# Performance work log

Hardware: AMD Instinct MI355X
Metric: run time of the kernel (lower is better)

The kernel has to match this reference:

```python
import jax, jax.numpy as jnp
import numpy as np

KS = 3          # deformable kernel size
PAD = 1         # zero padding
N = KS * KS     # sampling points per pixel
INC = 64
OUTC = 64


def _conv(x, w, stride, pad, groups):
    return jax.lax.conv_general_dilated(
        x, w, (stride, stride), ((pad, pad), (pad, pad)),
        feature_group_count=groups,
        dimension_numbers=('NCHW', 'OIHW', 'NCHW'))


def setup_inputs() -> dict:
    key = jax.random.key(0)
    k = jax.random.split(key, 5)
    b, h, w = 4, 128, 128
    x = jax.random.normal(k[0], (b, INC, h, w), jnp.float32)
    # SeparableConv2d params (bias=False throughout in source)
    p_dw = jax.random.normal(k[1], (INC, 1, 3, 3), jnp.float32) * 0.1     # p_conv depthwise 3x3 pad1
    p_pw = jax.random.normal(k[2], (2 * N, INC, 1, 1), jnp.float32) * 0.1  # p_conv pointwise -> 2N offsets
    c_dw = jax.random.normal(k[3], (INC, 1, KS, KS), jnp.float32) * 0.1    # conv depthwise k=ks stride=ks
    c_pw = jax.random.normal(k[4], (OUTC, INC, 1, 1), jnp.float32) * 0.1   # conv pointwise
    return {'x': x, 'p_dw': p_dw, 'p_pw': p_pw, 'c_dw': c_dw, 'c_pw': c_pw}


def reference(x, p_dw, p_pw, c_dw, c_pw):
    b, c, h, w = x.shape
    offset = _conv(_conv(x, p_dw, 1, 1, INC), p_pw, 1, 0, 1)   # [b, 2N, h, w]
    xp = jnp.pad(x, ((0, 0), (0, 0), (PAD, PAD), (PAD, PAD)))  # zero_padding
    Hp, Wp = h + 2 * PAD, w + 2 * PAD
    # p_n: kernel-relative offsets (row-major over ks x ks, 'ij' meshgrid)
    r = jnp.arange(-(KS - 1) // 2, (KS - 1) // 2 + 1, dtype=jnp.float32)
    pnx, pny = jnp.meshgrid(r, r, indexing='ij')
    p_n = jnp.concatenate([pnx.ravel(), pny.ravel()])[None, :, None, None]  # [1, 2N, 1, 1]
    # p_0: base grid, 1-indexed (accounts for padding), stride=1
    gx = jnp.arange(1, h + 1, dtype=jnp.float32)[None, None, :, None]
    gy = jnp.arange(1, w + 1, dtype=jnp.float32)[None, None, None, :]
    p0 = jnp.concatenate([jnp.broadcast_to(gx, (1, N, h, w)),
                          jnp.broadcast_to(gy, (1, N, h, w))], axis=1)      # [1, 2N, h, w]
    p = (p0 + p_n + offset).transpose(0, 2, 3, 1)                           # [b, h, w, 2N]
    px, py = p[..., :N], p[..., N:]
    fx, fy = jnp.floor(px), jnp.floor(py)
    ltx = jnp.clip(fx, 0, Hp - 1); lty = jnp.clip(fy, 0, Wp - 1)
    rbx = jnp.clip(fx + 1, 0, Hp - 1); rby = jnp.clip(fy + 1, 0, Wp - 1)
    pxc = jnp.clip(px, 0, Hp - 1); pyc = jnp.clip(py, 0, Wp - 1)
    # bilinear weights
    g_lt = (1 + (ltx - pxc)) * (1 + (lty - pyc))
    g_rb = (1 - (rbx - pxc)) * (1 - (rby - pyc))
    g_lb = (1 + (ltx - pxc)) * (1 - (rby - pyc))
    g_rt = (1 - (rbx - pxc)) * (1 + (lty - pyc))
    x_flat = xp.reshape(b, c, Hp * Wp)

    def gather(qx, qy):  # -> [b, c, h, w, N]
        idx = (qx * Wp + qy).astype(jnp.int32).reshape(b, 1, h * w * N)
        return jnp.take_along_axis(x_flat, idx, axis=2).reshape(b, c, h, w, N)

    x_off = (g_lt[:, None] * gather(ltx, lty) + g_rb[:, None] * gather(rbx, rby)
             + g_lb[:, None] * gather(ltx, rby) + g_rt[:, None] * gather(rbx, lty))
    # _reshape_x_offset: [b,c,h,w,N] -> [b,c,h*ks,w*ks]
    x_off = x_off.reshape(b, c, h, w, KS, KS).transpose(0, 1, 2, 4, 3, 5).reshape(b, c, h * KS, w * KS)
    # SeparableConv2d(inc, outc, k=ks, stride=ks)
    return _conv(_conv(x_off, c_dw, KS, 0, INC), c_pw, 1, 0, 1)
```

## Files before the change

kernel.cpp:

```cpp
#include <hip/hip_runtime.h>
#include <hip/hip_fp16.h>

#define Hdim 128
#define Wdim 128
#define Cdim 64
#define HW   (Hdim * Wdim)
#define NPIX (4 * HW)
#define NBLK (NPIX / 64)
#define NXCD 8
#define Hp 130
#define HWp (Hp * Hp)

typedef _Float16 v8h __attribute__((ext_vector_type(8)));
typedef float    v4f __attribute__((ext_vector_type(4)));

__device__ __forceinline__ int xcd_swizzle(int bid, int nblk) {
    return (bid % NXCD) * (nblk / NXCD) + bid / NXCD;
}


__global__ __launch_bounds__(512) void offset_geo_kernel(
    const float* __restrict__ x,
    const float* __restrict__ p_dw,
    const float* __restrict__ p_pw,
    __half* __restrict__ xt,
    unsigned int* __restrict__ geo)
{
    __shared__ float part[8][18][64];

    int lane = threadIdx.x & 63;
    int g    = threadIdx.x >> 6;
    int blk  = xcd_swizzle(blockIdx.x, NBLK);
    int pix0 = blk * 64;
    int pix  = pix0 + lane;
    int w = pix & (Wdim - 1);
    int h = (pix >> 7) & (Hdim - 1);
    int b = pix >> 14;

    {
        int gid = blockIdx.x * 512 + threadIdx.x;
        if (gid < 2064 * 8) {
            int rp  = gid >> 3, sub = gid & 7;
            int img = rp / 516, pos = rp - img * 516;
            int i, j;
            if (pos < 130)      { i = 0;   j = pos; }
            else if (pos < 260) { i = 129; j = pos - 130; }
            else { int p2 = pos - 260; i = 1 + (p2 >> 1); j = (p2 & 1) ? 129 : 0; }
            float4* dst = (float4*)(xt + ((size_t)img * HWp + i * Hp + j) * Cdim);
            dst[sub] = make_float4(0.f, 0.f, 0.f, 0.f);
        }
    }

    int   off9[9];
    float msk9[9];
#pragma unroll
    for (int dh = -1; dh <= 1; ++dh) {
#pragma unroll
        for (int dw = -1; dw <= 1; ++dw) {
            int tap = (dh + 1) * 3 + (dw + 1);
            int hh = h + dh, ww = w + dw;
            bool ok = (hh >= 0) & (hh < Hdim) & (ww >= 0) & (ww < Wdim);
            off9[tap] = ok ? hh * Wdim + ww : 0;
            msk9[tap] = ok ? 1.f : 0.f;
        }
    }

    float t[8], ctr[8];
#pragma unroll
    for (int i = 0; i < 8; ++i) {
        int c = g * 8 + i;
        const float* xb = x + (size_t)(b * Cdim + c) * HW;
        float s = 0.f;
#pragma unroll
        for (int tap = 0; tap < 9; ++tap) {
            float v = xb[off9[tap]] * msk9[tap];
            s += v * p_dw[c * 9 + tap];
        }
        t[i]   = s;
        ctr[i] = xb[h * Wdim + w];
    }

    {
        __half2 h0 = __floats2half2_rn(ctr[0], ctr[1]);
        __half2 h1 = __floats2half2_rn(ctr[2], ctr[3]);
        __half2 h2 = __floats2half2_rn(ctr[4], ctr[5]);
        __half2 h3 = __floats2half2_rn(ctr[6], ctr[7]);
        uint4 pk;
        pk.x = *(const unsigned int*)&h0;
        pk.y = *(const unsigned int*)&h1;
        pk.z = *(const unsigned int*)&h2;
        pk.w = *(const unsigned int*)&h3;
        size_t ppos = ((size_t)b * HWp + (h + 1) * Hp + (w + 1)) * Cdim + g * 8;
        *(uint4*)(xt + ppos) = pk;
    }

#pragma unroll
    for (int j = 0; j < 18; ++j) {
        float s = 0.f;
#pragma unroll
        for (int i = 0; i < 8; ++i)
            s += p_pw[j * Cdim + g * 8 + i] * t[i];
        part[g][j][lane] = s;
    }
    __syncthreads();

#pragma unroll
    for (int it = 0; it < 3; ++it) {
        int idx = threadIdx.x + it * 512;
        if (idx < 18 * 64) {
            int j = idx >> 6;
            int p = idx & 63;
            float s = part[0][j][p];
#pragma unroll
            for (int q = 1; q < 8; ++q) s += part[q][j][p];
            part[0][j][p] = s;
        }
    }
    __syncthreads();

#pragma unroll
    for (int it = 0; it < 2; ++it) {
        int idx = threadIdx.x + it * 512;
        if (idx < 9 * 64) {
            int k = idx >> 6;
            int p = idx & 63;
            int ppix = pix0 + p;
            int pw2 = ppix & (Wdim - 1);
            int ph2 = (ppix >> 7) & (Hdim - 1);

            float px = (float)(ph2 + 1) + (float)(k / 3 - 1) + part[0][k][p];
            float py = (float)(pw2 + 1) + (float)(k % 3 - 1) + part[0][k + 9][p];

            float fx = floorf(px), fy = floorf(py);
            float ltx = fminf(fmaxf(fx, 0.f), 129.f);
            float lty = fminf(fmaxf(fy, 0.f), 129.f);
            float rbx = fminf(fmaxf(fx + 1.f, 0.f), 129.f);
            float rby = fminf(fmaxf(fy + 1.f, 0.f), 129.f);
            float pxc = fminf(fmaxf(px, 0.f), 129.f);
            float pyc = fminf(fmaxf(py, 0.f), 129.f);

            float glt = (1.f + ltx - pxc) * (1.f + lty - pyc);
            float grb = (1.f - rbx + pxc) * (1.f - rby + pyc);
            float glb = (1.f + ltx - pxc) * (1.f - rby + pyc);
            float grt = (1.f - rbx + pxc) * (1.f + lty - pyc);

            int ix0 = (int)ltx, iy0 = (int)lty, ix1 = (int)rbx, iy1 = (int)rby;

            int base1, base2;
            if (iy1 == iy0 + 1) {
                base1 = ix0 * Hp + iy0;
                base2 = ix1 * Hp + iy0;
            } else {
                glt = glb = grt = grb = 0.f;
                base1 = base2 = 0;
            }

            __half2 wlo = __floats2half2_rn(glt, grt);
            __half2 whi = __floats2half2_rn(glb, grb);
            uint4 pk;
            pk.x = *(const unsigned int*)&wlo;
            pk.y = *(const unsigned int*)&whi;
            pk.z = (unsigned int)base1;
            pk.w = (unsigned int)base2;
            size_t e = ((size_t)blk * 8 + (p >> 3)) * 320 + (size_t)(k * 8 + (p & 7)) * 4;
            *(uint4*)(geo + e) = pk;
        }
    }
}

__global__ __launch_bounds__(512) void deform_kernel(
    const __half* __restrict__ xt,
    const float* __restrict__ c_dw,
    const float* __restrict__ c_pw,
    const int* __restrict__ geo,
    float* __restrict__ out)
{
    __shared__ _Float16 accs_h[64][72];
    __shared__ float    outD[64][69];

    int lane = threadIdx.x & 63;
    int c2   = lane & 31;
    bool lo  = lane < 32;
    int gu   = __builtin_amdgcn_readfirstlane(threadIdx.x >> 6);
    int blk  = xcd_swizzle(blockIdx.x, NBLK);
    int pix0 = blk * 64;
    int b    = pix0 >> 14;
    const __half* xb = xt + (size_t)b * HWp * Cdim;

    int gv0, gv1, gv2, gv3, gv4;
    {
        const int* gb = geo + ((size_t)blk * 8 + gu) * 320 + lane;
        gv0 = gb[0];   gv1 = gb[64];  gv2 = gb[128];
        gv3 = gb[192]; gv4 = gb[256];
    }
    float wkx9[9], wky9[9];
#pragma unroll
    for (int k = 0; k < 9; ++k) {
        wkx9[k] = c_dw[(2 * c2) * 9 + k];
        wky9[k] = c_dw[(2 * c2 + 1) * 9 + k];
    }

#define GV(r) ((r)==0?gv0:(r)==1?gv1:(r)==2?gv2:(r)==3?gv3:gv4)
#define RL(f) __builtin_amdgcn_readlane(GV((f) >> 6), (f) & 63)

    float2 acc2[8];
#pragma unroll
    for (int i = 0; i < 8; ++i) acc2[i] = make_float2(0.f, 0.f);

#pragma unroll
    for (int k = 0; k < 9; ++k) {
#pragma unroll
        for (int i = 0; i < 8; ++i) {
            const int f = (k * 8 + i) * 4;
            unsigned int d0 = (unsigned int)RL(f + 0);
            unsigned int d1 = (unsigned int)RL(f + 1);
            int bs1 = RL(f + 2);
            int bs2 = RL(f + 3);
            const unsigned int* p1 = (const unsigned int*)(xb + ((size_t)bs1 << 6));
            const unsigned int* p2 = (const unsigned int*)(xb + ((size_t)bs2 << 6));
            unsigned int v1 = p1[lane];
            unsigned int v2 = p2[lane];
            unsigned int wsu = lo ? d0 : d1;
            __half2 w12 = *(const __half2*)&wsu;
            __half2 v1h = *(const __half2*)&v1;
            __half2 v2h = *(const __half2*)&v2;
            __half2 tt = __hadd2(__hmul2(v1h, __half2half2(__low2half(w12))),
                                 __hmul2(v2h, __half2half2(__high2half(w12))));
            float2 tf = __half22float2(tt);
            acc2[i].x += wkx9[k] * tf.x;
            acc2[i].y += wky9[k] * tf.y;
        }
    }
#undef RL
#undef GV

#pragma unroll
    for (int i = 0; i < 8; ++i) {
        acc2[i].x += __shfl_xor(acc2[i].x, 32);
        acc2[i].y += __shfl_xor(acc2[i].y, 32);
    }
    if (lo) {
#pragma unroll
        for (int i = 0; i < 8; ++i) {
            __half2 hv = __floats2half2_rn(acc2[i].x, acc2[i].y);
            *(__half2*)&accs_h[gu * 8 + i][2 * c2] = hv;
        }
    }
    __syncthreads();

    {
        int pb = gu & 3;
        int ob = gu >> 2;
        int lr = lane & 15;
        int lg = lane >> 4;

        const v8h a0 = *(const v8h*)&accs_h[pb * 16 + lr][lg * 8];
        const v8h a1 = *(const v8h*)&accs_h[pb * 16 + lr][32 + lg * 8];

        v4f d0 = {0.f, 0.f, 0.f, 0.f}, d1 = {0.f, 0.f, 0.f, 0.f};
#pragma unroll
        for (int t = 0; t < 2; ++t) {
            int oc = ob * 32 + t * 16 + lr;
            const float* wr = c_pw + oc * Cdim + lg * 8;
            v8h b0, b1;
#pragma unroll
            for (int j = 0; j < 8; ++j) {
                b0[j] = (_Float16)wr[j];
                b1[j] = (_Float16)wr[32 + j];
            }
            if (t == 0) {
                d0 = __builtin_amdgcn_mfma_f32_16x16x32_f16(a0, b0, d0, 0, 0, 0);
                d0 = __builtin_amdgcn_mfma_f32_16x16x32_f16(a1, b1, d0, 0, 0, 0);
            } else {
                d1 = __builtin_amdgcn_mfma_f32_16x16x32_f16(a0, b0, d1, 0, 0, 0);
                d1 = __builtin_amdgcn_mfma_f32_16x16x32_f16(a1, b1, d1, 0, 0, 0);
            }
        }

#pragma unroll
        for (int r = 0; r < 4; ++r) {
            outD[pb * 16 + lg * 4 + r][ob * 32 + lr]      = d0[r];
            outD[pb * 16 + lg * 4 + r][ob * 32 + 16 + lr] = d1[r];
        }
    }
    __syncthreads();

    int pix = pix0 + lane;
    int hw  = pix & (HW - 1);
    size_t obase = (size_t)b * Cdim * HW + hw;
#pragma unroll
    for (int i = 0; i < 8; ++i)
        out[obase + (size_t)(gu * 8 + i) * HW] = outD[lane][gu * 8 + i];
}

extern "C" void kernel_launch(void* const* d_in, const int* in_sizes, int n_in,
                              void* d_out, int out_size, void* d_ws, size_t ws_size,
                              hipStream_t stream) {
    const float* x    = (const float*)d_in[0];
    const float* p_dw = (const float*)d_in[1];
    const float* p_pw = (const float*)d_in[2];
    const float* c_dw = (const float*)d_in[3];
    const float* c_pw = (const float*)d_in[4];
    float* out = (float*)d_out;

    __half* xt = (__half*)d_ws;
    unsigned int* geo = (unsigned int*)((char*)d_ws + (size_t)4 * HWp * Cdim * 2);

    offset_geo_kernel<<<dim3(NBLK), dim3(512), 0, stream>>>(x, p_dw, p_pw, xt, geo);
    deform_kernel<<<dim3(NBLK), dim3(512), 0, stream>>>(xt, c_dw, c_pw, (const int*)geo, out);
}
```

Before: 58.23 us.

## Split off transpose kernel and fuse offset computation into deform kernel

The NHWC fp16 transpose (plus border zeroing) now runs in its own small kernel that stages data through an LDS tile. The offset convolution and bilinear geometry are moved into the deform kernel, and the per-pixel geometry is passed through shared memory instead of a global buffer. This removes the global write and read of the geo array. The partial offset sums are also stored in fp16 in LDS, sharing space with later buffers, which may cost precision in the sampling offsets. The first kernel no longer reads x with the 9-tap pattern, but x is now read twice across the two kernels.

```diff
diff --git a/kernel.cpp b/kernel.cpp
--- a/kernel.cpp
+++ b/kernel.cpp
@@ -18,24 +18,19 @@
     return (bid % NXCD) * (nblk / NXCD) + bid / NXCD;
 }
 
-
-__global__ __launch_bounds__(512) void offset_geo_kernel(
+__global__ __launch_bounds__(512) void transpose_kernel(
     const float* __restrict__ x,
-    const float* __restrict__ p_dw,
-    const float* __restrict__ p_pw,
-    __half* __restrict__ xt,
-    unsigned int* __restrict__ geo)
+    __half* __restrict__ xt)
 {
-    __shared__ float part[8][18][64];
-
+    __shared__ float tile[64][65];
     int lane = threadIdx.x & 63;
     int g    = threadIdx.x >> 6;
     int blk  = xcd_swizzle(blockIdx.x, NBLK);
     int pix0 = blk * 64;
-    int pix  = pix0 + lane;
-    int w = pix & (Wdim - 1);
-    int h = (pix >> 7) & (Hdim - 1);
-    int b = pix >> 14;
+    int b    = pix0 >> 14;
+    int hw0  = pix0 & (HW - 1);
+    int h    = hw0 >> 7;
+    int w0   = hw0 & 127;
 
     {
         int gid = blockIdx.x * 512 + threadIdx.x;
@@ -51,6 +46,45 @@
         }
     }
 
+#pragma unroll
+    for (int i = 0; i < 8; ++i) {
+        int c = g * 8 + i;
+        tile[c][lane] = x[(size_t)(b * Cdim + c) * HW + hw0 + lane];
+    }
+    __syncthreads();
+#pragma unroll
+    for (int i = 0; i < 8; ++i) {
+        int p = g * 8 + i;
+        size_t ppos = ((size_t)b * HWp + (h + 1) * Hp + (w0 + 1 + p)) * Cdim + lane;
+        xt[ppos] = (__half)tile[lane][p];
+    }
+}
+
+__global__ __launch_bounds__(512) void fused_kernel(
+    const float* __restrict__ x,
+    const float* __restrict__ p_dw,
+    const float* __restrict__ p_pw,
+    const __half* __restrict__ xt,
+    const float* __restrict__ c_dw,
+    const float* __restrict__ c_pw,
+    float* __restrict__ out)
+{
+    __shared__ __align__(16) unsigned char smem[26880];
+    __shared__ __align__(16) unsigned int geoL[8][320];
+
+    auto part_h = (_Float16 (*)[18][64])smem;
+    auto accs_h = (_Float16 (*)[72])smem;
+    auto outD   = (float (*)[69])(smem + 9216);
+
+    int lane = threadIdx.x & 63;
+    int g    = threadIdx.x >> 6;
+    int blk  = xcd_swizzle(blockIdx.x, NBLK);
+    int pix0 = blk * 64;
+    int pix  = pix0 + lane;
+    int w = pix & (Wdim - 1);
+    int h = (pix >> 7) & (Hdim - 1);
+    int b = pix >> 14;
+
     int   off9[9];
     float msk9[9];
 #pragma unroll
@@ -65,33 +99,18 @@
         }
     }
 
-    float t[8], ctr[8];
+    float t[8];
 #pragma unroll
     for (int i = 0; i < 8; ++i) {
         int c = g * 8 + i;
-        const float* xb = x + (size_t)(b * Cdim + c) * HW;
+        const float* xb0 = x + (size_t)(b * Cdim + c) * HW;
         float s = 0.f;
 #pragma unroll
         for (int tap = 0; tap < 9; ++tap) {
-            float v = xb[off9[tap]] * msk9[tap];
+            float v = xb0[off9[tap]] * msk9[tap];
             s += v * p_dw[c * 9 + tap];
         }
-        t[i]   = s;
-        ctr[i] = xb[h * Wdim + w];
-    }
-
-    {
-        __half2 h0 = __floats2half2_rn(ctr[0], ctr[1]);
-        __half2 h1 = __floats2half2_rn(ctr[2], ctr[3]);
-        __half2 h2 = __floats2half2_rn(ctr[4], ctr[5]);
-        __half2 h3 = __floats2half2_rn(ctr[6], ctr[7]);
-        uint4 pk;
-        pk.x = *(const unsigned int*)&h0;
-        pk.y = *(const unsigned int*)&h1;
-        pk.z = *(const unsigned int*)&h2;
-        pk.w = *(const unsigned int*)&h3;
-        size_t ppos = ((size_t)b * HWp + (h + 1) * Hp + (w + 1)) * Cdim + g * 8;
-        *(uint4*)(xt + ppos) = pk;
+        t[i] = s;
     }
 
 #pragma unroll
@@ -100,7 +119,7 @@
 #pragma unroll
         for (int i = 0; i < 8; ++i)
             s += p_pw[j * Cdim + g * 8 + i] * t[i];
-        part[g][j][lane] = s;
+        part_h[g][j][lane] = (_Float16)s;
     }
     __syncthreads();
 
@@ -110,10 +129,10 @@
         if (idx < 18 * 64) {
             int j = idx >> 6;
             int p = idx & 63;
-            float s = part[0][j][p];
-#pragma unroll
-            for (int q = 1; q < 8; ++q) s += part[q][j][p];
-            part[0][j][p] = s;
+            float s = 0.f;
+#pragma unroll
+            for (int q = 0; q < 8; ++q) s += (float)part_h[q][j][p];
+            part_h[0][j][p] = (_Float16)s;
         }
     }
     __syncthreads();
@@ -128,8 +147,8 @@
             int pw2 = ppix & (Wdim - 1);
             int ph2 = (ppix >> 7) & (Hdim - 1);
 
-            float px = (float)(ph2 + 1) + (float)(k / 3 - 1) + part[0][k][p];
-            float py = (float)(pw2 + 1) + (float)(k % 3 - 1) + part[0][k + 9][p];
+            float px = (float)(ph2 + 1) + (float)(k / 3 - 1) + (float)part_h[0][k][p];
+            float py = (float)(pw2 + 1) + (float)(k % 3 - 1) + (float)part_h[0][k + 9][p];
 
             float fx = floorf(px), fy = floorf(py);
             float ltx = fminf(fmaxf(fx, 0.f), 129.f);
@@ -162,34 +181,19 @@
             pk.y = *(const unsigned int*)&whi;
             pk.z = (unsigned int)base1;
             pk.w = (unsigned int)base2;
-            size_t e = ((size_t)blk * 8 + (p >> 3)) * 320 + (size_t)(k * 8 + (p & 7)) * 4;
-            *(uint4*)(geo + e) = pk;
-        }
-    }
-}
-
-__global__ __launch_bounds__(512) void deform_kernel(
-    const __half* __restrict__ xt,
-    const float* __restrict__ c_dw,
-    const float* __restrict__ c_pw,
-    const int* __restrict__ geo,
-    float* __restrict__ out)
-{
-    __shared__ _Float16 accs_h[64][72];
-    __shared__ float    outD[64][69];
-
-    int lane = threadIdx.x & 63;
+            *(uint4*)&geoL[p >> 3][(k * 8 + (p & 7)) * 4] = pk;
+        }
+    }
+    __syncthreads();
+
     int c2   = lane & 31;
     bool lo  = lane < 32;
-    int gu   = __builtin_amdgcn_readfirstlane(threadIdx.x >> 6);
-    int blk  = xcd_swizzle(blockIdx.x, NBLK);
-    int pix0 = blk * 64;
-    int b    = pix0 >> 14;
+    int gu   = __builtin_amdgcn_readfirstlane(g);
     const __half* xb = xt + (size_t)b * HWp * Cdim;
 
     int gv0, gv1, gv2, gv3, gv4;
     {
-        const int* gb = geo + ((size_t)blk * 8 + gu) * 320 + lane;
+        const unsigned int* gb = &geoL[gu][0] + lane;
         gv0 = gb[0];   gv1 = gb[64];  gv2 = gb[128];
         gv3 = gb[192]; gv4 = gb[256];
     }
@@ -259,8 +263,8 @@
 
         v4f d0 = {0.f, 0.f, 0.f, 0.f}, d1 = {0.f, 0.f, 0.f, 0.f};
 #pragma unroll
-        for (int t = 0; t < 2; ++t) {
-            int oc = ob * 32 + t * 16 + lr;
+        for (int t2 = 0; t2 < 2; ++t2) {
+            int oc = ob * 32 + t2 * 16 + lr;
             const float* wr = c_pw + oc * Cdim + lg * 8;
             v8h b0, b1;
 #pragma unroll
@@ -268,7 +272,7 @@
                 b0[j] = (_Float16)wr[j];
                 b1[j] = (_Float16)wr[32 + j];
             }
-            if (t == 0) {
+            if (t2 == 0) {
                 d0 = __builtin_amdgcn_mfma_f32_16x16x32_f16(a0, b0, d0, 0, 0, 0);
                 d0 = __builtin_amdgcn_mfma_f32_16x16x32_f16(a1, b1, d0, 0, 0, 0);
             } else {
@@ -285,8 +289,7 @@
     }
     __syncthreads();
 
-    int pix = pix0 + lane;
-    int hw  = pix & (HW - 1);
+    int hw = pix & (HW - 1);
     size_t obase = (size_t)b * Cdim * HW + hw;
 #pragma unroll
     for (int i = 0; i < 8; ++i)
@@ -304,8 +307,7 @@
     float* out = (float*)d_out;
 
     __half* xt = (__half*)d_ws;
-    unsigned int* geo = (unsigned int*)((char*)d_ws + (size_t)4 * HWp * Cdim * 2);
-
-    offset_geo_kernel<<<dim3(NBLK), dim3(512), 0, stream>>>(x, p_dw, p_pw, xt, geo);
-    deform_kernel<<<dim3(NBLK), dim3(512), 0, stream>>>(xt, c_dw, c_pw, (const int*)geo, out);
+
+    transpose_kernel<<<dim3(NBLK), dim3(512), 0, stream>>>(x, xt);
+    fused_kernel<<<dim3(NBLK), dim3(512), 0, stream>>>(x, p_dw, p_pw, xt, c_dw, c_pw, out);
 }
```

After: 54.52 us. 1.07x faster.
